# Performance work log

Measured on AMD Instinct MI355X. Metric: run time of the kernel, lower is better.

Reference implementation:

```python
import jax, jax.numpy as jnp
import numpy as np

B, T, D, H = 2, 2048, 1024, 16
HD = D // H  # head dim = 64

def setup_inputs() -> dict:
    key = jax.random.key(0)
    k1, k2, k3 = jax.random.split(key, 3)
    x = jax.random.normal(k1, (B, T, D), dtype=jnp.float32)
    W_qkv = jax.random.normal(k2, (D, 3 * D), dtype=jnp.float32) * 0.02
    b_qkv = jax.random.normal(k3, (3 * D,), dtype=jnp.float32) * 0.02
    return {"x": x, "W_qkv": W_qkv, "b_qkv": b_qkv}

def reference(x, W_qkv, b_qkv):
    Bc, Tc, C = x.shape
    qkv = x @ W_qkv + b_qkv                     # [B,T,3D]
    q, k, v = jnp.split(qkv, 3, axis=-1)        # each [B,T,D]
    def to_heads(t):
        return t.reshape(Bc, Tc, H, HD).transpose(0, 2, 1, 3)  # [B,H,T,hd]
    q, k, v = to_heads(q), to_heads(k), to_heads(v)
    scale = 1.0 / jnp.sqrt(jnp.asarray(HD, dtype=x.dtype))
    att = jnp.einsum('bhqd,bhkd->bhqk', q, k) * scale  # [B,H,T,T]
    att = jax.nn.softmax(att, axis=-1)
    y = jnp.einsum('bhqk,bhkd->bhqd', att, v)          # [B,H,T,hd]
    return y.transpose(0, 2, 1, 3).reshape(Bc, Tc, C)
```

## Files before the change

### kernel.cpp

```cpp
#include <hip/hip_runtime.h>
#include <cstdint>

typedef unsigned short u16;
typedef __bf16 bf16x8 __attribute__((ext_vector_type(8)));
typedef float f32x4 __attribute__((ext_vector_type(4)));
typedef u16 u16x4 __attribute__((ext_vector_type(4)));
typedef u16 u16x8 __attribute__((ext_vector_type(8)));

static __device__ __forceinline__ u16 f2bf(float f) {
  return __builtin_bit_cast(u16, (__bf16)f);
}
static __device__ __forceinline__ float fexp2(float x) {
  float r;
  asm("v_exp_f32 %0, %1" : "=v"(r) : "v"(x));
  return r;
}

#define GLOAD16(gsrc, ldst) \
  __builtin_amdgcn_global_load_lds((const __attribute__((address_space(1))) void*)(gsrc), \
                                   (__attribute__((address_space(3))) void*)(ldst), 16, 0, 0)

#define WAIT_BAR_VM(n) do { \
    __builtin_amdgcn_sched_barrier(0); \
    asm volatile("s_waitcnt vmcnt(" #n ")" ::: "memory"); \
    __builtin_amdgcn_s_barrier(); \
    __builtin_amdgcn_sched_barrier(0); \
  } while (0)
#define WAIT_BAR_LGKM() do { \
    __builtin_amdgcn_sched_barrier(0); \
    asm volatile("s_waitcnt lgkmcnt(0)" ::: "memory"); \
    __builtin_amdgcn_s_barrier(); \
    __builtin_amdgcn_sched_barrier(0); \
  } while (0)


__global__ __launch_bounds__(256) void k_prep(const float* __restrict__ x,
                                              const float* __restrict__ W,
                                              u16* __restrict__ xbf,
                                              u16* __restrict__ Wt) {
  __shared__ __align__(16) u16 tile[64 * 72];
  int t = threadIdx.x;
  if (blockIdx.x < 2048) {
    int idx = blockIdx.x * 256 + t;
    const float4* xv = (const float4*)x;
    float4 a = xv[(size_t)idx * 2];
    float4 b = xv[(size_t)idx * 2 + 1];
    u16x8 o;
    o[0]=f2bf(a.x); o[1]=f2bf(a.y); o[2]=f2bf(a.z); o[3]=f2bf(a.w);
    o[4]=f2bf(b.x); o[5]=f2bf(b.y); o[6]=f2bf(b.z); o[7]=f2bf(b.w);
    *(u16x8*)(xbf + (size_t)idx * 8) = o;
    return;
  }
  int bid = blockIdx.x - 2048;
  int bk = bid & 15, bn = bid >> 4;
  int k0 = bk * 64, n0 = bn * 64;
  #pragma unroll
  for (int r = 0; r < 4; r++) {
    int id = r * 256 + t;
    int kl = id >> 4;
    int c  = (id & 15) * 4;
    float4 v = *(const float4*)(W + (size_t)(k0 + kl) * 3072 + n0 + c);
    u16x4 o; o[0]=f2bf(v.x); o[1]=f2bf(v.y); o[2]=f2bf(v.z); o[3]=f2bf(v.w);
    *(u16x4*)(tile + kl * 72 + c) = o;
  }
  __syncthreads();
  #pragma unroll
  for (int r = 0; r < 2; r++) {
    int id = r * 256 + t;
    int nl = id >> 3;
    int w  = id & 7;
    u16x8 o;
    #pragma unroll
    for (int i = 0; i < 8; i++) o[i] = tile[(w * 8 + i) * 72 + nl];
    *(u16x8*)(Wt + (size_t)(n0 + nl) * 1024 + k0 + w * 8) = o;
  }
}

__global__ __launch_bounds__(256, 2) void k_gemm_qkv(const u16* __restrict__ xbf,
                                                     const u16* __restrict__ wt,
                                                     const float* __restrict__ bias,
                                                     u16* __restrict__ qkv,
                                                     u16* __restrict__ vT) {
  __shared__ __align__(16) u16 As[2 * 128 * 64];
  __shared__ __align__(16) u16 Bs[2 * 192 * 64];
  int wg = blockIdx.x;
  int swz = (wg & 7) * 64 + (wg >> 3);
  int mt = swz >> 4, nt = swz & 15;
  int m0 = mt * 128, n0 = nt * 192;
  int t = threadIdx.x;
  int lane = t & 63, wid = t >> 6;
  int wm = wid >> 1, wn = wid & 1;
  int g = lane >> 4, li = lane & 15;

  f32x4 acc[4][6];
  #pragma unroll
  for (int i = 0; i < 4; i++)
    #pragma unroll
    for (int j = 0; j < 6; j++) acc[i][j] = (f32x4){0.f, 0.f, 0.f, 0.f};

  auto stage = [&](int kt, int buf) {
    char* ad = (char*)As + buf * 16384;
    char* bd = (char*)Bs + buf * 24576;
    #pragma unroll
    for (int i = 0; i < 4; i++) {
      int p = t + i * 256;
      int row = p >> 3, ug = (p & 7) ^ (row & 7);
      GLOAD16(xbf + (size_t)(m0 + row) * 1024 + kt * 64 + ug * 8, ad + p * 16);
    }
    #pragma unroll
    for (int i = 0; i < 6; i++) {
      int p = t + i * 256;
      int row = p >> 3, ug = (p & 7) ^ (row & 7);
      GLOAD16(wt + (size_t)(n0 + row) * 1024 + kt * 64 + ug * 8, bd + p * 16);
    }
  };

  stage(0, 0);
  for (int kt = 0; kt < 16; ++kt) {
    if (kt < 15) {
      stage(kt + 1, (kt & 1) ^ 1);
      WAIT_BAR_VM(10);
    } else {
      WAIT_BAR_VM(0);
    }
    const char* ab = (const char*)As + (kt & 1) * 16384;
    const char* bb = (const char*)Bs + (kt & 1) * 24576;

    #pragma unroll
    for (int kk = 0; kk < 2; ++kk) {
      bf16x8 af[4], bfr[6];
      #pragma unroll
      for (int mi = 0; mi < 4; mi++) {
        int row = wm * 64 + mi * 16 + li;
        int u = (kk * 4 + g) ^ (row & 7);
        af[mi] = *(const bf16x8*)(ab + row * 128 + u * 16);
      }
      #pragma unroll
      for (int ni = 0; ni < 6; ni++) {
        int row = wn * 96 + ni * 16 + li;
        int u = (kk * 4 + g) ^ (row & 7);
        bfr[ni] = *(const bf16x8*)(bb + row * 128 + u * 16);
      }
      __builtin_amdgcn_s_setprio(1);
      #pragma unroll
      for (int mi = 0; mi < 4; mi++)
        #pragma unroll
        for (int ni = 0; ni < 6; ni++)
          acc[mi][ni] = __builtin_amdgcn_mfma_f32_16x16x32_bf16(af[mi], bfr[ni], acc[mi][ni], 0, 0, 0);
      __builtin_amdgcn_s_setprio(0);
    }

    WAIT_BAR_LGKM();
  }

  int b = m0 >> 11;
  int tbase = m0 & 2047;
  #pragma unroll
  for (int ni = 0; ni < 6; ni++) {
    int col = n0 + wn * 96 + ni * 16 + li;
    float bv = bias[col];
    float sc = (col < 1024) ? 0.18033688011112042f : 1.0f;
    #pragma unroll
    for (int mi = 0; mi < 4; mi++) {
      int trow = tbase + wm * 64 + mi * 16 + g * 4;
      if (col < 2048) {
        #pragma unroll
        for (int j = 0; j < 4; j++) {
          float v = (acc[mi][ni][j] + bv) * sc;
          qkv[(size_t)(b * 2048 + trow + j) * 3072 + col] = f2bf(v);
        }
      } else {
        u16x4 o;
        #pragma unroll
        for (int j = 0; j < 4; j++) o[j] = f2bf(acc[mi][ni][j] + bv);
        *(u16x4*)(vT + ((size_t)(b * 1024 + (col - 2048))) * 2048 + trow) = o;
      }
    }
  }
}

__global__ __launch_bounds__(256, 2) void k_attn(const u16* __restrict__ qkv,
                                                 const u16* __restrict__ vT,
                                                 float* __restrict__ out) {
  __shared__ __align__(16) u16 smem[32768];
  int bid = blockIdx.x;
  int bh = bid & 31, qt = bid >> 5;
  int b = bh >> 4, h = bh & 15;
  int qbase = qt * 128;
  int t = threadIdx.x, lane = t & 63, wave = t >> 6;
  int g = lane >> 4, li = lane & 15;
  int kvHalf = wave >> 1, qh = wave & 1;

  bf16x8 q[4][2];
  #pragma unroll
  for (int qf = 0; qf < 4; qf++) {
    size_t qrow = (size_t)(b * 2048 + qbase + qh * 64 + qf * 16 + li) * 3072 + h * 64;
    q[qf][0] = *(const bf16x8*)(qkv + qrow + g * 8);
    q[qf][1] = *(const bf16x8*)(qkv + qrow + 32 + g * 8);
  }

  u16x8 ob;
  #pragma unroll
  for (int i = 0; i < 8; i++) ob[i] = 0x3F80;
  bf16x8 ones = __builtin_bit_cast(bf16x8, ob);

  f32x4 o[4][4];
  #pragma unroll
  for (int i = 0; i < 4; i++)
    #pragma unroll
    for (int j = 0; j < 4; j++) o[i][j] = (f32x4){0.f, 0.f, 0.f, 0.f};
  f32x4 la[4];
  #pragma unroll
  for (int i = 0; i < 4; i++) la[i] = (f32x4){0.f, 0.f, 0.f, 0.f};

  const u16* kbase_g = qkv + (size_t)(b * 2048) * 3072 + 1024 + h * 64;
  const u16* vbase_g = vT + (size_t)(bh * 64) * 2048;

  int kR[4], kU[4];
  size_t vO[4];
  #pragma unroll
  for (int i = 0; i < 4; i++) {
    int p = t + i * 256;
    int hf = p >> 9, p9 = p & 511;
    int kr = p9 >> 3;
    kR[i] = hf * 1024 + ((kr & 32) | ((kr & 16) >> 2) | (((kr >> 2) & 3) << 3) | (kr & 3));
    kU[i] = (p9 & 7) ^ (kr & 7);
    int d = p9 >> 3, u = p9 & 7;
    vO[i] = (size_t)d * 2048 + hf * 1024 + ((u ^ (d & 7)) * 8);
  }

  auto stage = [&](int key0, int buf) {
    char* kd = (char*)smem + buf * 32768;
    char* vd = kd + 16384;
    #pragma unroll
    for (int i = 0; i < 4; i++) {
      int p = t + i * 256;
      GLOAD16(kbase_g + (size_t)(key0 + kR[i]) * 3072 + kU[i] * 8, kd + p * 16);
      GLOAD16(vbase_g + vO[i] + key0, vd + p * 16);
    }
  };

  stage(0, 0);
  asm volatile("s_waitcnt vmcnt(0)" ::: "memory");
  __syncthreads();

  for (int ph = 0; ph < 16; ++ph) {
    const char* bufb = (const char*)smem + (ph & 1) * 32768;
    const char* kb = bufb + kvHalf * 8192;
    const char* vb = bufb + 16384 + kvHalf * 8192;

    if (ph < 15) {
      stage((ph + 1) * 64, (ph & 1) ^ 1);
      WAIT_BAR_VM(8);
    } else {
      WAIT_BAR_VM(0);
    }

    f32x4 s[4][4];
    int u0 = g ^ (li & 7);
    __builtin_amdgcn_s_setprio(1);
    #pragma unroll
    for (int st = 0; st < 4; ++st) {
      bf16x8 kf0 = *(const bf16x8*)(kb + (st * 16 + li) * 128 + u0 * 16);
      bf16x8 kf1 = *(const bf16x8*)(kb + (st * 16 + li) * 128 + (u0 ^ 4) * 16);
      #pragma unroll
      for (int qf = 0; qf < 4; qf++) {
        f32x4 z = (f32x4){0.f, 0.f, 0.f, 0.f};
        s[st][qf] = __builtin_amdgcn_mfma_f32_16x16x32_bf16(kf0, q[qf][0], z, 0, 0, 0);
        s[st][qf] = __builtin_amdgcn_mfma_f32_16x16x32_bf16(kf1, q[qf][1], s[st][qf], 0, 0, 0);
      }
    }
    __builtin_amdgcn_s_setprio(0);

    bf16x8 pb[4][2];
    #pragma unroll
    for (int qf = 0; qf < 4; qf++) {
      float p16[16];
      #pragma unroll
      for (int i = 0; i < 16; i++) p16[i] = fexp2(s[i >> 2][qf][i & 3]);
      #pragma unroll
      for (int c = 0; c < 2; c++)
        #pragma unroll
        for (int e = 0; e < 8; e++) pb[qf][c][e] = (__bf16)p16[c * 8 + e];
    }

    __builtin_amdgcn_s_setprio(1);
    #pragma unroll
    for (int qf = 0; qf < 4; qf++) {
      la[qf] = __builtin_amdgcn_mfma_f32_16x16x32_bf16(ones, pb[qf][0], la[qf], 0, 0, 0);
      la[qf] = __builtin_amdgcn_mfma_f32_16x16x32_bf16(ones, pb[qf][1], la[qf], 0, 0, 0);
    }
    #pragma unroll
    for (int c = 0; c < 2; c++) {
      #pragma unroll
      for (int dt = 0; dt < 4; dt++) {
        int d = dt * 16 + li;
        bf16x8 vf = *(const bf16x8*)(vb + d * 128 + (((c * 4 + g) ^ (d & 7)) << 4));
        #pragma unroll
        for (int qf = 0; qf < 4; qf++)
          o[qf][dt] = __builtin_amdgcn_mfma_f32_16x16x32_bf16(vf, pb[qf][c], o[qf][dt], 0, 0, 0);
      }
    }
    __builtin_amdgcn_s_setprio(0);

    WAIT_BAR_LGKM();
  }

  float* pO = (float*)smem;
  float* pL = (float*)((char*)smem + 32768);
  if (kvHalf) {
    #pragma unroll
    for (int qf = 0; qf < 4; qf++) {
      int qq = qh * 64 + qf * 16 + li;
      #pragma unroll
      for (int dt = 0; dt < 4; dt++) {
        int u = dt * 4 + g;
        *(f32x4*)((char*)pO + qq * 256 + ((u ^ (qq & 7)) << 4)) = o[qf][dt];
      }
      if (g == 0) pL[qq] = la[qf][0];
    }
  }
  __syncthreads();
  if (!kvHalf) {
    #pragma unroll
    for (int qf = 0; qf < 4; qf++) {
      int qq = qh * 64 + qf * 16 + li;
      float inv = 1.0f / (la[qf][0] + pL[qq]);
      size_t orow = (size_t)(b * 2048 + qbase + qq) * 1024 + h * 64;
      #pragma unroll
      for (int dt = 0; dt < 4; dt++) {
        int u = dt * 4 + g;
        f32x4 p2 = *(const f32x4*)((const char*)pO + qq * 256 + ((u ^ (qq & 7)) << 4));
        f32x4 r = (o[qf][dt] + p2) * inv;
        *(f32x4*)(out + orow + u * 4) = r;
      }
    }
  }
}

extern "C" void kernel_launch(void* const* d_in, const int* in_sizes, int n_in,
                              void* d_out, int out_size, void* d_ws, size_t ws_size,
                              hipStream_t stream) {
  const float* x    = (const float*)d_in[0];
  const float* W    = (const float*)d_in[1];
  const float* bias = (const float*)d_in[2];
  float* out = (float*)d_out;
  char* ws = (char*)d_ws;
  u16* xbf = (u16*)(ws + 0);
  u16* wt  = (u16*)(ws + 8388608);
  u16* qkv = (u16*)(ws + 14680064);
  u16* vt  = (u16*)(ws + 39845888);

  k_prep<<<2816, 256, 0, stream>>>(x, W, xbf, wt);
  k_gemm_qkv<<<512, 256, 0, stream>>>(xbf, wt, bias, qkv, vt);
  k_attn<<<512, 256, 0, stream>>>(qkv, vt, out);
}
```

Before: 82.05 us.

## Software-pipeline QK^T of next tile with exp of current tile, 4-stage KV ring

Restructures the attention loop into 32 phases of 32 keys each, computing the next tile's QK^T scores while exponentiating the current tile's scores, with the exp work interleaved between MFMA groups. K/V staging moves to a 4-buffer ring of smaller tiles, prefetched two phases ahead, with re-derived swizzles for the 64-byte V rows. This aims to overlap transcendental ALU work with matrix-core work and hide load latency. The cost is more score registers held live (two score sets) and more barriers per key, since tiles are half as large.

```diff
diff --git a/kernel.cpp b/kernel.cpp
--- a/kernel.cpp
+++ b/kernel.cpp
@@ -216,94 +216,129 @@
   const u16* kbase_g = qkv + (size_t)(b * 2048) * 3072 + 1024 + h * 64;
   const u16* vbase_g = vT + (size_t)(bh * 64) * 2048;
 
-  int kR[4], kU[4];
-  size_t vO[4];
-  #pragma unroll
-  for (int i = 0; i < 4; i++) {
+  size_t kSrc[2], vSrc[2];
+  int kDst[2], vDst[2];
+  #pragma unroll
+  for (int i = 0; i < 2; i++) {
     int p = t + i * 256;
-    int hf = p >> 9, p9 = p & 511;
-    int kr = p9 >> 3;
-    kR[i] = hf * 1024 + ((kr & 32) | ((kr & 16) >> 2) | (((kr >> 2) & 3) << 3) | (kr & 3));
-    kU[i] = (p9 & 7) ^ (kr & 7);
-    int d = p9 >> 3, u = p9 & 7;
-    vO[i] = (size_t)d * 2048 + hf * 1024 + ((u ^ (d & 7)) * 8);
+    int hf = p >> 8, p8 = p & 255;
+    int row = p8 >> 3, u = p8 & 7;
+    int kperm = ((row & 16) >> 2) | (((row >> 2) & 3) << 3) | (row & 3);
+    kSrc[i] = (size_t)(hf * 1024 + kperm) * 3072 + (size_t)((u ^ (row & 7)) * 8);
+    kDst[i] = p * 16;
+    int d = p8 >> 2, uv = p8 & 3;
+    vSrc[i] = (size_t)d * 2048 + hf * 1024 + (size_t)((uv ^ ((d >> 1) & 3)) * 8);
+    vDst[i] = p * 16;
   }
 
   auto stage = [&](int key0, int buf) {
-    char* kd = (char*)smem + buf * 32768;
-    char* vd = kd + 16384;
-    #pragma unroll
-    for (int i = 0; i < 4; i++) {
-      int p = t + i * 256;
-      GLOAD16(kbase_g + (size_t)(key0 + kR[i]) * 3072 + kU[i] * 8, kd + p * 16);
-      GLOAD16(vbase_g + vO[i] + key0, vd + p * 16);
+    char* kd = (char*)smem + buf * 16384;
+    char* vd = kd + 8192;
+    #pragma unroll
+    for (int i = 0; i < 2; i++) {
+      GLOAD16(kbase_g + (size_t)key0 * 3072 + kSrc[i], kd + kDst[i]);
+      GLOAD16(vbase_g + vSrc[i] + key0, vd + vDst[i]);
     }
   };
 
+  f32x4 sA[2][4], sB[2][4];
+  int u0 = g ^ (li & 7);
+
+  auto qkc = [&](const char* kb, f32x4 (&S)[2][4]) {
+    #pragma unroll
+    for (int st = 0; st < 2; ++st) {
+      bf16x8 kf0 = *(const bf16x8*)(kb + (st * 16 + li) * 128 + u0 * 16);
+      bf16x8 kf1 = *(const bf16x8*)(kb + (st * 16 + li) * 128 + (u0 ^ 4) * 16);
+      #pragma unroll
+      for (int qf = 0; qf < 4; qf++) {
+        f32x4 z = (f32x4){0.f, 0.f, 0.f, 0.f};
+        S[st][qf] = __builtin_amdgcn_mfma_f32_16x16x32_bf16(kf0, q[qf][0], z, 0, 0, 0);
+        S[st][qf] = __builtin_amdgcn_mfma_f32_16x16x32_bf16(kf1, q[qf][1], S[st][qf], 0, 0, 0);
+      }
+    }
+  };
+
+  auto phase = [&](int i, f32x4 (&Sc)[2][4], f32x4 (&Sn)[2][4]) {
+    if (i < 30) {
+      stage((i + 2) * 32, (i + 2) & 3);
+      WAIT_BAR_VM(4);
+    } else {
+      WAIT_BAR_VM(0);
+    }
+
+    float p16[4][8];
+    if (i < 31) {
+      const char* kbn = (const char*)smem + ((i + 1) & 3) * 16384 + kvHalf * 4096;
+      __builtin_amdgcn_s_setprio(1);
+      bf16x8 kf0 = *(const bf16x8*)(kbn + li * 128 + u0 * 16);
+      bf16x8 kf1 = *(const bf16x8*)(kbn + li * 128 + (u0 ^ 4) * 16);
+      #pragma unroll
+      for (int qf = 0; qf < 4; qf++) {
+        f32x4 z = (f32x4){0.f, 0.f, 0.f, 0.f};
+        Sn[0][qf] = __builtin_amdgcn_mfma_f32_16x16x32_bf16(kf0, q[qf][0], z, 0, 0, 0);
+        Sn[0][qf] = __builtin_amdgcn_mfma_f32_16x16x32_bf16(kf1, q[qf][1], Sn[0][qf], 0, 0, 0);
+      }
+      __builtin_amdgcn_s_setprio(0);
+      #pragma unroll
+      for (int qf = 0; qf < 2; qf++)
+        #pragma unroll
+        for (int e = 0; e < 8; e++) p16[qf][e] = fexp2(Sc[e >> 2][qf][e & 3]);
+      __builtin_amdgcn_s_setprio(1);
+      bf16x8 kf2 = *(const bf16x8*)(kbn + (16 + li) * 128 + u0 * 16);
+      bf16x8 kf3 = *(const bf16x8*)(kbn + (16 + li) * 128 + (u0 ^ 4) * 16);
+      #pragma unroll
+      for (int qf = 0; qf < 4; qf++) {
+        f32x4 z = (f32x4){0.f, 0.f, 0.f, 0.f};
+        Sn[1][qf] = __builtin_amdgcn_mfma_f32_16x16x32_bf16(kf2, q[qf][0], z, 0, 0, 0);
+        Sn[1][qf] = __builtin_amdgcn_mfma_f32_16x16x32_bf16(kf3, q[qf][1], Sn[1][qf], 0, 0, 0);
+      }
+      __builtin_amdgcn_s_setprio(0);
+      #pragma unroll
+      for (int qf = 2; qf < 4; qf++)
+        #pragma unroll
+        for (int e = 0; e < 8; e++) p16[qf][e] = fexp2(Sc[e >> 2][qf][e & 3]);
+    } else {
+      #pragma unroll
+      for (int qf = 0; qf < 4; qf++)
+        #pragma unroll
+        for (int e = 0; e < 8; e++) p16[qf][e] = fexp2(Sc[e >> 2][qf][e & 3]);
+    }
+
+    bf16x8 pb[4];
+    #pragma unroll
+    for (int qf = 0; qf < 4; qf++)
+      #pragma unroll
+      for (int e = 0; e < 8; e++) pb[qf][e] = (__bf16)p16[qf][e];
+
+    const char* vb = (const char*)smem + (i & 3) * 16384 + 8192 + kvHalf * 4096;
+    __builtin_amdgcn_s_setprio(1);
+    #pragma unroll
+    for (int qf = 0; qf < 4; qf++)
+      la[qf] = __builtin_amdgcn_mfma_f32_16x16x32_bf16(ones, pb[qf], la[qf], 0, 0, 0);
+    #pragma unroll
+    for (int dt = 0; dt < 4; dt++) {
+      int d = dt * 16 + li;
+      bf16x8 vf = *(const bf16x8*)(vb + d * 64 + ((g ^ ((d >> 1) & 3)) << 4));
+      #pragma unroll
+      for (int qf = 0; qf < 4; qf++)
+        o[qf][dt] = __builtin_amdgcn_mfma_f32_16x16x32_bf16(vf, pb[qf], o[qf][dt], 0, 0, 0);
+    }
+    __builtin_amdgcn_s_setprio(0);
+
+    WAIT_BAR_LGKM();
+  };
+
   stage(0, 0);
+  stage(32, 1);
   asm volatile("s_waitcnt vmcnt(0)" ::: "memory");
   __syncthreads();
-
-  for (int ph = 0; ph < 16; ++ph) {
-    const char* bufb = (const char*)smem + (ph & 1) * 32768;
-    const char* kb = bufb + kvHalf * 8192;
-    const char* vb = bufb + 16384 + kvHalf * 8192;
-
-    if (ph < 15) {
-      stage((ph + 1) * 64, (ph & 1) ^ 1);
-      WAIT_BAR_VM(8);
-    } else {
-      WAIT_BAR_VM(0);
-    }
-
-    f32x4 s[4][4];
-    int u0 = g ^ (li & 7);
-    __builtin_amdgcn_s_setprio(1);
-    #pragma unroll
-    for (int st = 0; st < 4; ++st) {
-      bf16x8 kf0 = *(const bf16x8*)(kb + (st * 16 + li) * 128 + u0 * 16);
-      bf16x8 kf1 = *(const bf16x8*)(kb + (st * 16 + li) * 128 + (u0 ^ 4) * 16);
-      #pragma unroll
-      for (int qf = 0; qf < 4; qf++) {
-        f32x4 z = (f32x4){0.f, 0.f, 0.f, 0.f};
-        s[st][qf] = __builtin_amdgcn_mfma_f32_16x16x32_bf16(kf0, q[qf][0], z, 0, 0, 0);
-        s[st][qf] = __builtin_amdgcn_mfma_f32_16x16x32_bf16(kf1, q[qf][1], s[st][qf], 0, 0, 0);
-      }
-    }
-    __builtin_amdgcn_s_setprio(0);
-
-    bf16x8 pb[4][2];
-    #pragma unroll
-    for (int qf = 0; qf < 4; qf++) {
-      float p16[16];
-      #pragma unroll
-      for (int i = 0; i < 16; i++) p16[i] = fexp2(s[i >> 2][qf][i & 3]);
-      #pragma unroll
-      for (int c = 0; c < 2; c++)
-        #pragma unroll
-        for (int e = 0; e < 8; e++) pb[qf][c][e] = (__bf16)p16[c * 8 + e];
-    }
-
-    __builtin_amdgcn_s_setprio(1);
-    #pragma unroll
-    for (int qf = 0; qf < 4; qf++) {
-      la[qf] = __builtin_amdgcn_mfma_f32_16x16x32_bf16(ones, pb[qf][0], la[qf], 0, 0, 0);
-      la[qf] = __builtin_amdgcn_mfma_f32_16x16x32_bf16(ones, pb[qf][1], la[qf], 0, 0, 0);
-    }
-    #pragma unroll
-    for (int c = 0; c < 2; c++) {
-      #pragma unroll
-      for (int dt = 0; dt < 4; dt++) {
-        int d = dt * 16 + li;
-        bf16x8 vf = *(const bf16x8*)(vb + d * 128 + (((c * 4 + g) ^ (d & 7)) << 4));
-        #pragma unroll
-        for (int qf = 0; qf < 4; qf++)
-          o[qf][dt] = __builtin_amdgcn_mfma_f32_16x16x32_bf16(vf, pb[qf][c], o[qf][dt], 0, 0, 0);
-      }
-    }
-    __builtin_amdgcn_s_setprio(0);
-
-    WAIT_BAR_LGKM();
+  __builtin_amdgcn_s_setprio(1);
+  qkc((const char*)smem + kvHalf * 4096, sA);
+  __builtin_amdgcn_s_setprio(0);
+
+  for (int ii = 0; ii < 16; ++ii) {
+    phase(2 * ii, sA, sB);
+    phase(2 * ii + 1, sB, sA);
   }
 
   float* pO = (float*)smem;
```

New measurement: 81.99 us. Within noise of the previous version (-0.1%).

## Restructure attention into barrier-free per-wave KV pipelines with smaller blocks

Applied to the files above, without the earlier changes.

The attention kernel now uses 128-thread blocks over 64 queries, so the launch has twice as many blocks. Each of the two waves owns half of the key range and its own K/V LDS region. The block-wide barriers in the main loop are replaced by per-wave waitcnts, and the next K and V tiles are issued separately so they overlap with the V and QK compute. The row-sum MFMA against a ones vector is replaced by VALU adds plus a final lane shuffle reduction. This is meant to remove barrier stalls and extra MFMA work, but each wave now has a single LDS buffer, so loads can stall on compute, and Q is reloaded by more blocks.

```diff
diff --git a/kernel.cpp b/kernel.cpp
--- a/kernel.cpp
+++ b/kernel.cpp
@@ -30,6 +30,17 @@
     __builtin_amdgcn_sched_barrier(0); \
     asm volatile("s_waitcnt lgkmcnt(0)" ::: "memory"); \
     __builtin_amdgcn_s_barrier(); \
+    __builtin_amdgcn_sched_barrier(0); \
+  } while (0)
+
+#define WV_VM(n) do { \
+    __builtin_amdgcn_sched_barrier(0); \
+    asm volatile("s_waitcnt vmcnt(" #n ")" ::: "memory"); \
+    __builtin_amdgcn_sched_barrier(0); \
+  } while (0)
+#define WV_LGKM() do { \
+    __builtin_amdgcn_sched_barrier(0); \
+    asm volatile("s_waitcnt lgkmcnt(0)" ::: "memory"); \
     __builtin_amdgcn_sched_barrier(0); \
   } while (0)
 
@@ -179,123 +190,109 @@
   }
 }
 
-__global__ __launch_bounds__(256, 2) void k_attn(const u16* __restrict__ qkv,
+__global__ __launch_bounds__(128, 2) void k_attn(const u16* __restrict__ qkv,
                                                  const u16* __restrict__ vT,
                                                  float* __restrict__ out) {
-  __shared__ __align__(16) u16 smem[32768];
+  __shared__ __align__(16) u16 smem[16384];
   int bid = blockIdx.x;
   int bh = bid & 31, qt = bid >> 5;
   int b = bh >> 4, h = bh & 15;
-  int qbase = qt * 128;
+  int qbase = qt * 64;
   int t = threadIdx.x, lane = t & 63, wave = t >> 6;
   int g = lane >> 4, li = lane & 15;
-  int kvHalf = wave >> 1, qh = wave & 1;
 
   bf16x8 q[4][2];
   #pragma unroll
   for (int qf = 0; qf < 4; qf++) {
-    size_t qrow = (size_t)(b * 2048 + qbase + qh * 64 + qf * 16 + li) * 3072 + h * 64;
+    size_t qrow = (size_t)(b * 2048 + qbase + qf * 16 + li) * 3072 + h * 64;
     q[qf][0] = *(const bf16x8*)(qkv + qrow + g * 8);
     q[qf][1] = *(const bf16x8*)(qkv + qrow + 32 + g * 8);
   }
 
-  u16x8 ob;
-  #pragma unroll
-  for (int i = 0; i < 8; i++) ob[i] = 0x3F80;
-  bf16x8 ones = __builtin_bit_cast(bf16x8, ob);
-
   f32x4 o[4][4];
   #pragma unroll
   for (int i = 0; i < 4; i++)
     #pragma unroll
     for (int j = 0; j < 4; j++) o[i][j] = (f32x4){0.f, 0.f, 0.f, 0.f};
-  f32x4 la[4];
-  #pragma unroll
-  for (int i = 0; i < 4; i++) la[i] = (f32x4){0.f, 0.f, 0.f, 0.f};
-
-  const u16* kbase_g = qkv + (size_t)(b * 2048) * 3072 + 1024 + h * 64;
-  const u16* vbase_g = vT + (size_t)(bh * 64) * 2048;
-
-  int kR[4], kU[4];
-  size_t vO[4];
-  #pragma unroll
-  for (int i = 0; i < 4; i++) {
-    int p = t + i * 256;
-    int hf = p >> 9, p9 = p & 511;
-    int kr = p9 >> 3;
-    kR[i] = hf * 1024 + ((kr & 32) | ((kr & 16) >> 2) | (((kr >> 2) & 3) << 3) | (kr & 3));
-    kU[i] = (p9 & 7) ^ (kr & 7);
-    int d = p9 >> 3, u = p9 & 7;
-    vO[i] = (size_t)d * 2048 + hf * 1024 + ((u ^ (d & 7)) * 8);
-  }
-
-  auto stage = [&](int key0, int buf) {
-    char* kd = (char*)smem + buf * 32768;
-    char* vd = kd + 16384;
-    #pragma unroll
-    for (int i = 0; i < 4; i++) {
-      int p = t + i * 256;
-      GLOAD16(kbase_g + (size_t)(key0 + kR[i]) * 3072 + kU[i] * 8, kd + p * 16);
-      GLOAD16(vbase_g + vO[i] + key0, vd + p * 16);
-    }
+  float la[4] = {0.f, 0.f, 0.f, 0.f};
+
+  const u16* kbase_g = qkv + (size_t)(b * 2048 + wave * 1024) * 3072 + 1024 + h * 64;
+  const u16* vbase_g = vT + (size_t)(bh * 64) * 2048 + wave * 1024;
+
+  int r0 = lane >> 3, uu = lane & 7;
+  int kuo = (uu ^ (r0 & 7)) * 8;
+  int kR[8];
+  #pragma unroll
+  for (int i = 0; i < 8; i++) {
+    int r = r0 + 8 * i;
+    kR[i] = (r & 32) | ((r & 16) >> 2) | (((r >> 2) & 3) << 3) | (r & 3);
+  }
+  size_t vS0 = (size_t)r0 * 2048 + kuo;
+  char* kd = (char*)smem + wave * 16384;
+  char* vd = kd + 8192;
+
+  auto stageK = [&](int key0) {
+    #pragma unroll
+    for (int i = 0; i < 8; i++)
+      GLOAD16(kbase_g + (size_t)(key0 + kR[i]) * 3072 + kuo, kd + (lane + i * 64) * 16);
   };
-
-  stage(0, 0);
-  asm volatile("s_waitcnt vmcnt(0)" ::: "memory");
-  __syncthreads();
-
+  auto stageV = [&](int key0) {
+    #pragma unroll
+    for (int i = 0; i < 8; i++)
+      GLOAD16(vbase_g + vS0 + (size_t)i * 16384 + key0, vd + (lane + i * 64) * 16);
+  };
+
+  stageK(0);
+  stageV(0);
+  WV_VM(0);
+
+  int u0 = g ^ (li & 7);
+
+  #pragma unroll 1
   for (int ph = 0; ph < 16; ++ph) {
-    const char* bufb = (const char*)smem + (ph & 1) * 32768;
-    const char* kb = bufb + kvHalf * 8192;
-    const char* vb = bufb + 16384 + kvHalf * 8192;
-
-    if (ph < 15) {
-      stage((ph + 1) * 64, (ph & 1) ^ 1);
-      WAIT_BAR_VM(8);
-    } else {
-      WAIT_BAR_VM(0);
-    }
-
-    f32x4 s[4][4];
-    int u0 = g ^ (li & 7);
+    if (ph > 0) WV_VM(8);
+
+    bf16x8 pb[4][2];
+    #pragma unroll
+    for (int b2 = 0; b2 < 2; ++b2) {
+      f32x4 s[2][4];
+      __builtin_amdgcn_s_setprio(1);
+      #pragma unroll
+      for (int st = 0; st < 2; ++st) {
+        int row = (b2 * 2 + st) * 16 + li;
+        bf16x8 kf0 = *(const bf16x8*)(kd + row * 128 + u0 * 16);
+        bf16x8 kf1 = *(const bf16x8*)(kd + row * 128 + (u0 ^ 4) * 16);
+        #pragma unroll
+        for (int qf = 0; qf < 4; qf++) {
+          f32x4 z = (f32x4){0.f, 0.f, 0.f, 0.f};
+          s[st][qf] = __builtin_amdgcn_mfma_f32_16x16x32_bf16(kf0, q[qf][0], z, 0, 0, 0);
+          s[st][qf] = __builtin_amdgcn_mfma_f32_16x16x32_bf16(kf1, q[qf][1], s[st][qf], 0, 0, 0);
+        }
+      }
+      __builtin_amdgcn_s_setprio(0);
+      #pragma unroll
+      for (int qf = 0; qf < 4; qf++) {
+        float p8[8];
+        #pragma unroll
+        for (int e = 0; e < 8; e++) p8[e] = fexp2(s[e >> 2][qf][e & 3]);
+        la[qf] += ((p8[0] + p8[1]) + (p8[2] + p8[3])) + ((p8[4] + p8[5]) + (p8[6] + p8[7]));
+        #pragma unroll
+        for (int e = 0; e < 8; e++) pb[qf][b2][e] = (__bf16)p8[e];
+      }
+    }
+
+    WV_LGKM();
+    if (ph < 15) stageK((ph + 1) * 64);
+
+    if (ph < 15) WV_VM(8); else WV_VM(0);
+
     __builtin_amdgcn_s_setprio(1);
-    #pragma unroll
-    for (int st = 0; st < 4; ++st) {
-      bf16x8 kf0 = *(const bf16x8*)(kb + (st * 16 + li) * 128 + u0 * 16);
-      bf16x8 kf1 = *(const bf16x8*)(kb + (st * 16 + li) * 128 + (u0 ^ 4) * 16);
-      #pragma unroll
-      for (int qf = 0; qf < 4; qf++) {
-        f32x4 z = (f32x4){0.f, 0.f, 0.f, 0.f};
-        s[st][qf] = __builtin_amdgcn_mfma_f32_16x16x32_bf16(kf0, q[qf][0], z, 0, 0, 0);
-        s[st][qf] = __builtin_amdgcn_mfma_f32_16x16x32_bf16(kf1, q[qf][1], s[st][qf], 0, 0, 0);
-      }
-    }
-    __builtin_amdgcn_s_setprio(0);
-
-    bf16x8 pb[4][2];
-    #pragma unroll
-    for (int qf = 0; qf < 4; qf++) {
-      float p16[16];
-      #pragma unroll
-      for (int i = 0; i < 16; i++) p16[i] = fexp2(s[i >> 2][qf][i & 3]);
-      #pragma unroll
-      for (int c = 0; c < 2; c++)
-        #pragma unroll
-        for (int e = 0; e < 8; e++) pb[qf][c][e] = (__bf16)p16[c * 8 + e];
-    }
-
-    __builtin_amdgcn_s_setprio(1);
-    #pragma unroll
-    for (int qf = 0; qf < 4; qf++) {
-      la[qf] = __builtin_amdgcn_mfma_f32_16x16x32_bf16(ones, pb[qf][0], la[qf], 0, 0, 0);
-      la[qf] = __builtin_amdgcn_mfma_f32_16x16x32_bf16(ones, pb[qf][1], la[qf], 0, 0, 0);
-    }
     #pragma unroll
     for (int c = 0; c < 2; c++) {
       #pragma unroll
       for (int dt = 0; dt < 4; dt++) {
         int d = dt * 16 + li;
-        bf16x8 vf = *(const bf16x8*)(vb + d * 128 + (((c * 4 + g) ^ (d & 7)) << 4));
+        bf16x8 vf = *(const bf16x8*)(vd + d * 128 + (((c * 4 + g) ^ (d & 7)) << 4));
         #pragma unroll
         for (int qf = 0; qf < 4; qf++)
           o[qf][dt] = __builtin_amdgcn_mfma_f32_16x16x32_bf16(vf, pb[qf][c], o[qf][dt], 0, 0, 0);
@@ -303,29 +300,37 @@
     }
     __builtin_amdgcn_s_setprio(0);
 
-    WAIT_BAR_LGKM();
+    WV_LGKM();
+    if (ph < 15) stageV((ph + 1) * 64);
+  }
+
+  #pragma unroll
+  for (int qf = 0; qf < 4; qf++) {
+    la[qf] += __shfl_xor(la[qf], 16);
+    la[qf] += __shfl_xor(la[qf], 32);
   }
 
   float* pO = (float*)smem;
-  float* pL = (float*)((char*)smem + 32768);
-  if (kvHalf) {
+  float* pL = (float*)((char*)smem + 16384);
+  __syncthreads();
+  if (wave) {
     #pragma unroll
     for (int qf = 0; qf < 4; qf++) {
-      int qq = qh * 64 + qf * 16 + li;
+      int qq = qf * 16 + li;
       #pragma unroll
       for (int dt = 0; dt < 4; dt++) {
         int u = dt * 4 + g;
         *(f32x4*)((char*)pO + qq * 256 + ((u ^ (qq & 7)) << 4)) = o[qf][dt];
       }
-      if (g == 0) pL[qq] = la[qf][0];
+      if (g == 0) pL[qq] = la[qf];
     }
   }
   __syncthreads();
-  if (!kvHalf) {
+  if (!wave) {
     #pragma unroll
     for (int qf = 0; qf < 4; qf++) {
-      int qq = qh * 64 + qf * 16 + li;
-      float inv = 1.0f / (la[qf][0] + pL[qq]);
+      int qq = qf * 16 + li;
+      float inv = 1.0f / (la[qf] + pL[qq]);
       size_t orow = (size_t)(b * 2048 + qbase + qq) * 1024 + h * 64;
       #pragma unroll
       for (int dt = 0; dt < 4; dt++) {
@@ -353,5 +358,5 @@
 
   k_prep<<<2816, 256, 0, stream>>>(x, W, xbf, wt);
   k_gemm_qkv<<<512, 256, 0, stream>>>(xbf, wt, bias, qkv, vt);
-  k_attn<<<512, 256, 0, stream>>>(qkv, vt, out);
-}
+  k_attn<<<1024, 128, 0, stream>>>(qkv, vt, out);
+}
```

After: 84.00 us. 1.02x slower.

## Double attention query tile to 256 rows with 8 waves sharing K/V staging

Applied to the files above, without the earlier changes.

The attention kernel now launches 256 blocks of 512 threads. Each block covers 256 query rows with 8 waves: 4 query quarters times 2 KV halves. Each K/V tile staged into LDS is therefore reused by twice as many query rows, which halves global K/V traffic and the number of staging loads per thread. The trade-off is half as many blocks (a single wave of work on the GPU), a larger LDS footprint for the final cross-half reduction, and a different per-CU occupancy balance.

```diff
diff --git a/kernel.cpp b/kernel.cpp
--- a/kernel.cpp
+++ b/kernel.cpp
@@ -179,22 +179,22 @@
   }
 }
 
-__global__ __launch_bounds__(256, 2) void k_attn(const u16* __restrict__ qkv,
+__global__ __launch_bounds__(512, 2) void k_attn(const u16* __restrict__ qkv,
                                                  const u16* __restrict__ vT,
                                                  float* __restrict__ out) {
-  __shared__ __align__(16) u16 smem[32768];
+  __shared__ __align__(16) u16 smem[33280];
   int bid = blockIdx.x;
   int bh = bid & 31, qt = bid >> 5;
   int b = bh >> 4, h = bh & 15;
-  int qbase = qt * 128;
+  int qbase = qt * 256;
   int t = threadIdx.x, lane = t & 63, wave = t >> 6;
   int g = lane >> 4, li = lane & 15;
-  int kvHalf = wave >> 1, qh = wave & 1;
+  int kvHalf = wave >> 2, qq4 = wave & 3;
 
   bf16x8 q[4][2];
   #pragma unroll
   for (int qf = 0; qf < 4; qf++) {
-    size_t qrow = (size_t)(b * 2048 + qbase + qh * 64 + qf * 16 + li) * 3072 + h * 64;
+    size_t qrow = (size_t)(b * 2048 + qbase + qq4 * 64 + qf * 16 + li) * 3072 + h * 64;
     q[qf][0] = *(const bf16x8*)(qkv + qrow + g * 8);
     q[qf][1] = *(const bf16x8*)(qkv + qrow + 32 + g * 8);
   }
@@ -216,28 +216,30 @@
   const u16* kbase_g = qkv + (size_t)(b * 2048) * 3072 + 1024 + h * 64;
   const u16* vbase_g = vT + (size_t)(bh * 64) * 2048;
 
-  int kR[4], kU[4];
-  size_t vO[4];
-  #pragma unroll
-  for (int i = 0; i < 4; i++) {
-    int p = t + i * 256;
+  size_t kSrc[2], vSrc[2];
+  int kDst[2], vDst[2];
+  #pragma unroll
+  for (int i = 0; i < 2; i++) {
+    int p = t + i * 512;
     int hf = p >> 9, p9 = p & 511;
-    int kr = p9 >> 3;
-    kR[i] = hf * 1024 + ((kr & 32) | ((kr & 16) >> 2) | (((kr >> 2) & 3) << 3) | (kr & 3));
-    kU[i] = (p9 & 7) ^ (kr & 7);
-    int d = p9 >> 3, u = p9 & 7;
-    vO[i] = (size_t)d * 2048 + hf * 1024 + ((u ^ (d & 7)) * 8);
+    int row = p9 >> 3, ch = p9 & 7;
+    int pr = (row & 32) | ((row & 16) >> 2) | (((row >> 2) & 3) << 3) | (row & 3);
+    kSrc[i] = (size_t)(hf * 1024 + pr) * 3072 + (size_t)((ch ^ (row & 7)) * 8);
+    kDst[i] = p * 16;
+    int pv = p;
+    pv = t + (i + 2) * 512 - 1024;
+    int hfv = pv >> 9, p9v = pv & 511;
+    int d = p9v >> 3, chv = p9v & 7;
+    vSrc[i] = (size_t)d * 2048 + (size_t)(hfv * 1024) + (size_t)((chv ^ (d & 7)) * 8);
+    vDst[i] = 16384 + pv * 16;
   }
 
   auto stage = [&](int key0, int buf) {
-    char* kd = (char*)smem + buf * 32768;
-    char* vd = kd + 16384;
-    #pragma unroll
-    for (int i = 0; i < 4; i++) {
-      int p = t + i * 256;
-      GLOAD16(kbase_g + (size_t)(key0 + kR[i]) * 3072 + kU[i] * 8, kd + p * 16);
-      GLOAD16(vbase_g + vO[i] + key0, vd + p * 16);
-    }
+    char* base = (char*)smem + buf * 32768;
+    GLOAD16(kbase_g + (size_t)key0 * 3072 + kSrc[0], base + kDst[0]);
+    GLOAD16(kbase_g + (size_t)key0 * 3072 + kSrc[1], base + kDst[1]);
+    GLOAD16(vbase_g + vSrc[0] + key0, base + vDst[0]);
+    GLOAD16(vbase_g + vSrc[1] + key0, base + vDst[1]);
   };
 
   stage(0, 0);
@@ -246,12 +248,12 @@
 
   for (int ph = 0; ph < 16; ++ph) {
     const char* bufb = (const char*)smem + (ph & 1) * 32768;
-    const char* kb = bufb + kvHalf * 8192;
-    const char* vb = bufb + 16384 + kvHalf * 8192;
+    const char* kd = bufb + kvHalf * 8192;
+    const char* vd = bufb + 16384 + kvHalf * 8192;
 
     if (ph < 15) {
       stage((ph + 1) * 64, (ph & 1) ^ 1);
-      WAIT_BAR_VM(8);
+      WAIT_BAR_VM(4);
     } else {
       WAIT_BAR_VM(0);
     }
@@ -261,8 +263,8 @@
     __builtin_amdgcn_s_setprio(1);
     #pragma unroll
     for (int st = 0; st < 4; ++st) {
-      bf16x8 kf0 = *(const bf16x8*)(kb + (st * 16 + li) * 128 + u0 * 16);
-      bf16x8 kf1 = *(const bf16x8*)(kb + (st * 16 + li) * 128 + (u0 ^ 4) * 16);
+      bf16x8 kf0 = *(const bf16x8*)(kd + (st * 16 + li) * 128 + u0 * 16);
+      bf16x8 kf1 = *(const bf16x8*)(kd + (st * 16 + li) * 128 + (u0 ^ 4) * 16);
       #pragma unroll
       for (int qf = 0; qf < 4; qf++) {
         f32x4 z = (f32x4){0.f, 0.f, 0.f, 0.f};
@@ -295,7 +297,7 @@
       #pragma unroll
       for (int dt = 0; dt < 4; dt++) {
         int d = dt * 16 + li;
-        bf16x8 vf = *(const bf16x8*)(vb + d * 128 + (((c * 4 + g) ^ (d & 7)) << 4));
+        bf16x8 vf = *(const bf16x8*)(vd + d * 128 + (((c * 4 + g) ^ (d & 7)) << 4));
         #pragma unroll
         for (int qf = 0; qf < 4; qf++)
           o[qf][dt] = __builtin_amdgcn_mfma_f32_16x16x32_bf16(vf, pb[qf][c], o[qf][dt], 0, 0, 0);
@@ -306,31 +308,34 @@
     WAIT_BAR_LGKM();
   }
 
-  float* pO = (float*)smem;
-  float* pL = (float*)((char*)smem + 32768);
-  if (kvHalf) {
+  auto oAddr = [&](int a, int qq, int u) -> char* {
+    return (char*)smem + a * 16384 + qq * 256 + ((u ^ (qq & 7)) << 4);
+  };
+  __syncthreads();
+  if (wave >= 4) {
+    int a = wave - 4;
+    float* laA = (float*)((char*)smem + 65536 + a * 256);
     #pragma unroll
     for (int qf = 0; qf < 4; qf++) {
-      int qq = qh * 64 + qf * 16 + li;
+      int qq = qf * 16 + li;
+      #pragma unroll
+      for (int dt = 0; dt < 4; dt++)
+        *(f32x4*)oAddr(a, qq, dt * 4 + g) = o[qf][dt];
+      if (g == 0) laA[qq] = la[qf][0];
+    }
+  }
+  __syncthreads();
+  if (wave < 4) {
+    float* laA = (float*)((char*)smem + 65536 + wave * 256);
+    #pragma unroll
+    for (int qf = 0; qf < 4; qf++) {
+      int qq = qf * 16 + li;
+      float inv = 1.0f / (la[qf][0] + laA[qq]);
+      size_t orow = (size_t)(b * 2048 + qbase + wave * 64 + qq) * 1024 + h * 64;
       #pragma unroll
       for (int dt = 0; dt < 4; dt++) {
         int u = dt * 4 + g;
-        *(f32x4*)((char*)pO + qq * 256 + ((u ^ (qq & 7)) << 4)) = o[qf][dt];
-      }
-      if (g == 0) pL[qq] = la[qf][0];
-    }
-  }
-  __syncthreads();
-  if (!kvHalf) {
-    #pragma unroll
-    for (int qf = 0; qf < 4; qf++) {
-      int qq = qh * 64 + qf * 16 + li;
-      float inv = 1.0f / (la[qf][0] + pL[qq]);
-      size_t orow = (size_t)(b * 2048 + qbase + qq) * 1024 + h * 64;
-      #pragma unroll
-      for (int dt = 0; dt < 4; dt++) {
-        int u = dt * 4 + g;
-        f32x4 p2 = *(const f32x4*)((const char*)pO + qq * 256 + ((u ^ (qq & 7)) << 4));
+        f32x4 p2 = *(const f32x4*)oAddr(wave, qq, u);
         f32x4 r = (o[qf][dt] + p2) * inv;
         *(f32x4*)(out + orow + u * 4) = r;
       }
@@ -353,5 +358,5 @@
 
   k_prep<<<2816, 256, 0, stream>>>(x, W, xbf, wt);
   k_gemm_qkv<<<512, 256, 0, stream>>>(xbf, wt, bias, qkv, vt);
-  k_attn<<<512, 256, 0, stream>>>(qkv, vt, out);
-}
+  k_attn<<<256, 512, 0, stream>>>(qkv, vt, out);
+}
```

Measured after the change: 81.39 us. About the same (-0.8%).
